# Kernel optimization log

Measured on AMD Instinct MI355X. Metric: run time of the kernel, lower is better.

The kernel has to match this reference:

```python
import jax, jax.numpy as jnp
import numpy as np

B, T, D, H, R = 8, 2048, 1024, 1024, 128
R_MAX, R_MIN, MAX_PHASE = 1.0, 0.0, 6.28


def setup_inputs() -> dict:
    key = jax.random.key(0)
    ks = jax.random.split(key, 10)
    x = jax.random.normal(ks[0], (B, T, D), dtype=jnp.float32)
    # nu_log / theta_log init as in the torch module constructor
    u1 = jax.random.uniform(ks[1], (H,), dtype=jnp.float32)
    inner = u1 * (R_MAX ** 2 - R_MIN ** 2) + R_MIN ** 2
    nu_log = jnp.log(-0.5 * jnp.log(inner + 1e-6) + 1e-6)
    u2 = jax.random.uniform(ks[2], (H,), dtype=jnp.float32)
    theta_log = jnp.log(MAX_PHASE * u2 + 1e-6)
    U1 = jax.random.normal(ks[3], (D, R), dtype=jnp.float32) / np.sqrt(D)
    U2 = jax.random.normal(ks[4], (D, R), dtype=jnp.float32) / np.sqrt(D)
    V1 = jax.random.normal(ks[5], (R, H), dtype=jnp.float32) / np.sqrt(R)
    V2 = jax.random.normal(ks[6], (R, H), dtype=jnp.float32) / np.sqrt(R)
    hc1_init = jax.random.normal(ks[7], (B, H), dtype=jnp.float32) * 0.1
    hc2_init = jax.random.normal(ks[8], (B, H), dtype=jnp.float32) * 0.1
    return {"x": x, "nu_log": nu_log, "theta_log": theta_log,
            "U1": U1, "U2": U2, "V1": V1, "V2": V2,
            "hc1_init": hc1_init, "hc2_init": hc2_init}


def _combine(left, right):
    # Compose complex rotations g+i*phi and accumulate rotated biases:
    # A = A_r * A_l ; b = A_r * b_l + b_r  (complex arithmetic in real pairs)
    gL, pL, bxL, byL = left
    gR, pR, bxR, byR = right
    g_new = gR * gL - pR * pL
    p_new = pR * gL + gR * pL
    bx_new = gR * bxL - pR * byL + bxR
    by_new = pR * bxL + gR * byL + byR
    return (g_new, p_new, bx_new, by_new)


def reference(x, nu_log, theta_log, U1, U2, V1, V2, hc1_init, hc2_init):
    r = jnp.exp(-jnp.exp(nu_log))                      # [H]
    theta = jnp.exp(theta_log)                         # [H]
    g = r * jnp.cos(theta)
    phi = r * jnp.sin(theta)
    gamma = jnp.sqrt(jnp.clip(1.0 - r * r, 0.0))
    # Low-rank input projections: [B,T,D] -> [B,T,R] -> [B,T,H]
    u1 = jnp.einsum('btr,rh->bth', jnp.einsum('btd,dr->btr', x, U1), V1)
    u2 = jnp.einsum('btr,rh->bth', jnp.einsum('btd,dr->btr', x, U2), V2)
    bx = u1 * gamma                                    # [B,T,H]
    by = u2 * gamma
    Bb, Tt, Hh = bx.shape
    gT = jnp.broadcast_to(g, (Bb, Tt, Hh))
    pT = jnp.broadcast_to(phi, (Bb, Tt, Hh))
    # Inclusive parallel scan over time (Hillis-Steele equivalent)
    gA, pA, Bx, By = jax.lax.associative_scan(_combine, (gT, pT, bx, by), axis=1)
    # c_t = A_t * c_0 + B_t  (complex mul in real pairs)
    c0x = hc1_init[:, None, :]
    c0y = hc2_init[:, None, :]
    c1 = gA * c0x - pA * c0y + Bx                      # [B,T,H]
    c2 = pA * c0x + gA * c0y + By
    # activation = identity (default nn.Identity in the module)
    y = jnp.concatenate([c1, c2], axis=-1)             # [B,T,2H]
    return y, c1[:, -1, :], c2[:, -1, :]
```

## Files before the change

kernel.cpp:

```cpp
#include <hip/hip_runtime.h>


using u16 = unsigned short;
using frag_ab = __attribute__((ext_vector_type(8))) short;
using frag_cd = __attribute__((ext_vector_type(4))) float;

__device__ __forceinline__ u16 f2bf(float f) {
    union { float f; unsigned u; } v; v.f = f;
    unsigned r = v.u + 0x7FFFu + ((v.u >> 16) & 1u);
    return (u16)(r >> 16);
}
__device__ __forceinline__ float bf2f(u16 s) {
    union { unsigned u; float f; } v; v.u = ((unsigned)s) << 16;
    return v.f;
}
__device__ __forceinline__ frag_cd mfma16(frag_ab a, frag_ab b, frag_cd c) {
    return __builtin_amdgcn_mfma_f32_16x16x32_bf16(a, b, c, 0, 0, 0);
}

__global__ __launch_bounds__(256) void k0_pack(
    const float* __restrict__ U1, const float* __restrict__ U2,
    const float* __restrict__ V1, const float* __restrict__ V2,
    u16* __restrict__ Ubfp, u16* __restrict__ Vt)
{
    int idx = blockIdx.x * 256 + threadIdx.x;
    if (idx < 32768) {
        int kg = idx & 127, n = idx >> 7;
        const float* Us = (n < 128) ? U1 : U2;
        int col = n & 127;
        u16 tmp[8];
#pragma unroll
        for (int j = 0; j < 8; ++j)
            tmp[j] = f2bf(Us[(size_t)(kg * 8 + j) * 128 + col]);
        *(uint4*)&Ubfp[((size_t)(kg >> 3) * 256 + n) * 64 + (kg & 7) * 8] = *(uint4*)tmp;
    } else {
        int i2 = idx - 32768;
        int kg = i2 & 15, h = (i2 >> 4) & 1023, br = i2 >> 14;
        const float* Vs = br ? V2 : V1;
        u16 tmp[8];
#pragma unroll
        for (int j = 0; j < 8; ++j)
            tmp[j] = f2bf(Vs[(size_t)(kg * 8 + j) * 1024 + h]);
        *(uint4*)&Vt[((size_t)br * 1024 + h) * 128 + kg * 8] = *(uint4*)tmp;
    }
}

__global__ __launch_bounds__(256) void k1_gemm(
    const float* __restrict__ x, const u16* __restrict__ Ubfp, u16* __restrict__ xu)
{
    __shared__ __align__(16) u16 Alds[4 * 520];
    __shared__ __align__(16) u16 Blds[32 * 520];
    u16* Tlds = Blds;
    const int tid = threadIdx.x;
    const int m0 = blockIdx.x * 32;
    const int wave = tid >> 6, lane = tid & 63;
    const int lm = lane & 15, q = lane >> 4;
    const int rowA = tid >> 3, kcA = tid & 7;
    frag_cd acc[2][4] = {};

    const float* xsrc = x + (size_t)(m0 + rowA) * 1024 + kcA * 8;
    const char* bsrc = (const char*)Ubfp;
    char* bdst = (char*)Blds;

    float4 pA0 = *(const float4*)xsrc;
    float4 pA1 = *(const float4*)(xsrc + 4);

    for (int kt = 0; kt < 16; ++kt) {
        {
            u16 ap[8] = { f2bf(pA0.x), f2bf(pA0.y), f2bf(pA0.z), f2bf(pA0.w),
                          f2bf(pA1.x), f2bf(pA1.y), f2bf(pA1.z), f2bf(pA1.w) };
            *(uint4*)&Alds[(rowA >> 3) * 520 + (rowA & 7) * 64 + kcA * 8] = *(uint4*)ap;
        }
#pragma unroll
        for (int i = 0; i < 8; ++i) {
            int blk = wave * 8 + i;
            __builtin_amdgcn_global_load_lds(
                (const __attribute__((address_space(1))) void*)(bsrc + (size_t)kt * 32768 + blk * 1024 + lane * 16),
                (__attribute__((address_space(3))) void*)(bdst + blk * 1040), 16, 0, 0);
        }
        __syncthreads();
        if (kt + 1 < 16) {
            pA0 = *(const float4*)(xsrc + (kt + 1) * 64);
            pA1 = *(const float4*)(xsrc + (kt + 1) * 64 + 4);
        }
        frag_ab a[2], b[4];
#pragma unroll
        for (int ksub = 0; ksub < 2; ++ksub) {
#pragma unroll
            for (int m4 = 0; m4 < 2; ++m4) {
                int ra = m4 * 16 + lm;
                a[m4] = *(const frag_ab*)&Alds[(ra >> 3) * 520 + (ra & 7) * 64 + ksub * 32 + q * 8];
            }
#pragma unroll
            for (int n4 = 0; n4 < 4; ++n4) {
                int nb = wave * 64 + n4 * 16 + lm;
                b[n4] = *(const frag_ab*)&Blds[(nb >> 3) * 520 + (nb & 7) * 64 + ksub * 32 + q * 8];
            }
#pragma unroll
            for (int m4 = 0; m4 < 2; ++m4)
#pragma unroll
                for (int n4 = 0; n4 < 4; ++n4)
                    acc[m4][n4] = mfma16(a[m4], b[n4], acc[m4][n4]);
        }
        __syncthreads();
    }
    const int rb = q * 4;
#pragma unroll
    for (int m4 = 0; m4 < 2; ++m4)
#pragma unroll
        for (int n4 = 0; n4 < 4; ++n4)
#pragma unroll
            for (int i = 0; i < 4; ++i) {
                int m = m4 * 16 + rb + i;
                int n = wave * 64 + n4 * 16 + lm;
                Tlds[m * 256 + n] = f2bf(acc[m4][n4][i]);
            }
    __syncthreads();
#pragma unroll
    for (int p = 0; p < 4; ++p) {
        int m = p * 8 + (tid >> 5);
        int c = tid & 31;
        uint4 v = *(const uint4*)&Tlds[m * 256 + c * 8];
        *(uint4*)&xu[(size_t)(m0 + m) * 256 + c * 8] = v;
    }
}

__device__ __forceinline__ void compute_u_tile(
    const u16* __restrict__ xu, const u16* __restrict__ Vt,
    int t0, int h0, int tid, u16* smem)
{
    u16* xulds = smem;
    u16* Vlds  = smem + 16640;
    const int wave = tid >> 6, lane = tid & 63;
    const int lm = lane & 15, q = lane >> 4;
    const int wrow = wave >> 1, wcol = wave & 1;

    const char* gsrc = (const char*)xu + (size_t)t0 * 512;
    char* lb = (char*)xulds;
#pragma unroll
    for (int i = 0; i < 8; ++i) {
        int blk = wave * 8 + i;
        __builtin_amdgcn_global_load_lds(
            (const __attribute__((address_space(1))) void*)(gsrc + blk * 1024 + lane * 16),
            (__attribute__((address_space(3))) void*)(lb + blk * 1040), 16, 0, 0);
    }

    const int nV = tid & 63, wV = tid >> 6;
    const int ra0 = wrow * 32 + lm, ra1 = ra0 + 16;
    const int ba0 = (ra0 >> 1) * 520 + (ra0 & 1) * 256;
    const int ba1 = (ra1 >> 1) * 520 + (ra1 & 1) * 256;
    const int nb0 = wcol * 32 + lm, nb1 = nb0 + 16;
    frag_cd acc[2][2][2] = {};
#pragma unroll
    for (int br = 0; br < 2; ++br) {
#pragma unroll
        for (int ii = 0; ii < 4; ++ii) {
            int g = wV * 4 + ii;
            uint4 v = *(const uint4*)&Vt[((size_t)br * 1024 + h0 + nV) * 128 + g * 8];
            *(uint4*)&Vlds[nV * 128 + (g ^ (nV & 15)) * 8] = v;
        }
        __syncthreads();
#pragma unroll
        for (int ks = 0; ks < 4; ++ks) {
            int koff = br * 128 + ks * 32 + q * 8;
            frag_ab a0 = *(const frag_ab*)&xulds[ba0 + koff];
            frag_ab a1 = *(const frag_ab*)&xulds[ba1 + koff];
            int gb = ks * 4 + q;
            frag_ab b0 = *(const frag_ab*)&Vlds[nb0 * 128 + (gb ^ (nb0 & 15)) * 8];
            frag_ab b1 = *(const frag_ab*)&Vlds[nb1 * 128 + (gb ^ (nb1 & 15)) * 8];
            acc[br][0][0] = mfma16(a0, b0, acc[br][0][0]);
            acc[br][0][1] = mfma16(a0, b1, acc[br][0][1]);
            acc[br][1][0] = mfma16(a1, b0, acc[br][1][0]);
            acc[br][1][1] = mfma16(a1, b1, acc[br][1][1]);
        }
        __syncthreads();
    }
    const int rb = q * 4;
#pragma unroll
    for (int br = 0; br < 2; ++br)
#pragma unroll
        for (int fr = 0; fr < 2; ++fr)
#pragma unroll
            for (int fc = 0; fc < 2; ++fc)
#pragma unroll
                for (int i = 0; i < 4; ++i) {
                    int tt = wrow * 32 + fr * 16 + rb + i;
                    int hh = wcol * 32 + fc * 16 + lm;
                    smem[br * 4352 + tt * 68 + hh] = f2bf(acc[br][fr][fc][i]);
                }
    __syncthreads();
}

__device__ __forceinline__ void lambda_of(const float* nu_log, const float* theta_log,
                                          int h, float& g, float& ph, float& gam)
{
    float rr = expf(-expf(nu_log[h]));
    float th = expf(theta_log[h]);
    g = rr * cosf(th);
    ph = rr * sinf(th);
    gam = sqrtf(fmaxf(1.0f - rr * rr, 0.0f));
}

__global__ __launch_bounds__(256, 3) void k2_agg(
    const u16* __restrict__ xu, const u16* __restrict__ Vt,
    const float* __restrict__ nu_log, const float* __restrict__ theta_log,
    float2* __restrict__ agg)
{
    __shared__ __align__(16) u16 smem[24832];
    const int tid = threadIdx.x;
    const int h0 = blockIdx.x * 64;
    const int t0 = blockIdx.y * 64;
    compute_u_tile(xu, Vt, t0, h0, tid, smem);

    const int hl = tid & 63, sc = tid >> 6;
    const int h = h0 + hl;
    float g, ph, gam;
    lambda_of(nu_log, theta_log, h, g, ph, gam);
    float bx = 0.f, by = 0.f;
#pragma unroll
    for (int j = 0; j < 16; ++j) {
        int tt = sc * 16 + j;
        float u1 = bf2f(smem[tt * 68 + hl]);
        float u2 = bf2f(smem[4352 + tt * 68 + hl]);
        float ex = gam * u1, ey = gam * u2;
        float nx = fmaf(g, bx, fmaf(-ph, by, ex));
        float ny = fmaf(ph, bx, fmaf(g, by, ey));
        bx = nx; by = ny;
    }
    const int b = t0 >> 11;
    const int nc = ((t0 & 2047) >> 4) + sc;
    agg[((size_t)b * 128 + nc) * 1024 + h] = make_float2(bx, by);
}

__global__ __launch_bounds__(64) void k3_scan(
    float2* __restrict__ agg_carry, const float* __restrict__ nu_log,
    const float* __restrict__ theta_log, const float* __restrict__ hc1,
    const float* __restrict__ hc2)
{
    const int idx = blockIdx.x * 64 + threadIdx.x;
    const int b = idx >> 10, h = idx & 1023;
    float g, ph, gam;
    lambda_of(nu_log, theta_log, h, g, ph, gam);
    float ax = g, ay = ph;
#pragma unroll
    for (int i = 0; i < 4; ++i) { float nx = ax * ax - ay * ay, ny = 2.f * ax * ay; ax = nx; ay = ny; }
    float cx = hc1[idx], cy = hc2[idx];
    float2* acp = agg_carry + (size_t)b * 128 * 1024 + h;
#pragma unroll 8
    for (int c = 0; c < 128; ++c) {
        float2 a = acp[(size_t)c * 1024];
        acp[(size_t)c * 1024] = make_float2(cx, cy);
        float nx = fmaf(ax, cx, fmaf(-ay, cy, a.x));
        float ny = fmaf(ay, cx, fmaf(ax, cy, a.y));
        cx = nx; cy = ny;
    }
}

__global__ __launch_bounds__(256, 3) void k4_apply(
    const u16* __restrict__ xu, const u16* __restrict__ Vt,
    const float* __restrict__ nu_log, const float* __restrict__ theta_log,
    const float2* __restrict__ carries, float* __restrict__ out)
{
    __shared__ __align__(16) u16 smem[24832];
    const int tid = threadIdx.x;
    const int h0 = blockIdx.x * 64;
    const int t0 = blockIdx.y * 64;
    compute_u_tile(xu, Vt, t0, h0, tid, smem);

    const int hl = tid & 63, sc = tid >> 6;
    const int h = h0 + hl;
    float g, ph, gam;
    lambda_of(nu_log, theta_log, h, g, ph, gam);
    const int b = t0 >> 11;
    const int tloc = t0 & 2047;
    const int nc = (tloc >> 4) + sc;
    float2 cin = carries[((size_t)b * 128 + nc) * 1024 + h];
    float cx = cin.x, cy = cin.y;
    float* yb = out + (size_t)b * (2048 * 2048);
#pragma unroll
    for (int j = 0; j < 16; ++j) {
        int tt = sc * 16 + j;
        float u1 = bf2f(smem[tt * 68 + hl]);
        float u2 = bf2f(smem[4352 + tt * 68 + hl]);
        float ex = gam * u1, ey = gam * u2;
        float nx = fmaf(g, cx, fmaf(-ph, cy, ex));
        float ny = fmaf(ph, cx, fmaf(g, cy, ey));
        cx = nx; cy = ny;
        int t = tloc + tt;
        yb[(size_t)t * 2048 + h] = cx;
        yb[(size_t)t * 2048 + 1024 + h] = cy;
    }
    if (tloc + sc * 16 == 2032) {
        out[(size_t)33554432 + (size_t)b * 1024 + h] = cx;
        out[(size_t)33554432 + 8192 + (size_t)b * 1024 + h] = cy;
    }
}

extern "C" void kernel_launch(void* const* d_in, const int* in_sizes, int n_in,
                              void* d_out, int out_size, void* d_ws, size_t ws_size,
                              hipStream_t stream) {
    const float* x         = (const float*)d_in[0];
    const float* nu_log    = (const float*)d_in[1];
    const float* theta_log = (const float*)d_in[2];
    const float* U1        = (const float*)d_in[3];
    const float* U2        = (const float*)d_in[4];
    const float* V1        = (const float*)d_in[5];
    const float* V2        = (const float*)d_in[6];
    const float* hc1       = (const float*)d_in[7];
    const float* hc2       = (const float*)d_in[8];

    u16*    xu   = (u16*)d_ws;
    float2* agg  = (float2*)((char*)d_ws + (size_t)8 * 1024 * 1024);
    u16*    Vt   = (u16*)((char*)d_ws + (size_t)16 * 1024 * 1024);
    u16*    Ubfp = (u16*)((char*)d_ws + (size_t)16 * 1024 * 1024 + 512 * 1024);

    k0_pack<<<256, 256, 0, stream>>>(U1, U2, V1, V2, Ubfp, Vt);
    k1_gemm<<<512, 256, 0, stream>>>(x, Ubfp, xu);
    k2_agg<<<dim3(16, 256), 256, 0, stream>>>(xu, Vt, nu_log, theta_log, agg);
    k3_scan<<<128, 64, 0, stream>>>(agg, nu_log, theta_log, hc1, hc2);
    k4_apply<<<dim3(16, 256), 256, 0, stream>>>(xu, Vt, nu_log, theta_log, agg, (float*)d_out);
}
```

Measured before the change: 278.5 us.

## Cache bf16 u tiles from aggregate pass and reuse them in apply kernel

The aggregate kernel now writes its computed bf16 u tile (XOR-swizzled in shared memory instead of padded) to a workspace buffer. The apply kernel no longer recomputes the low-rank projection GEMM. It bulk-loads the cached tiles straight into LDS with global_load_lds and processes 256 timesteps by 4 hidden units per thread, using float4 output stores. This removes the duplicated MFMA work in the apply pass at the cost of extra workspace traffic (32 MB write plus read).

```diff
diff --git a/kernel.cpp b/kernel.cpp
--- a/kernel.cpp
+++ b/kernel.cpp
@@ -17,6 +17,7 @@
 __device__ __forceinline__ frag_cd mfma16(frag_ab a, frag_ab b, frag_cd c) {
     return __builtin_amdgcn_mfma_f32_16x16x32_bf16(a, b, c, 0, 0, 0);
 }
+__device__ __forceinline__ int ukey(int tt) { return (((tt >> 2) ^ (tt >> 4)) & 3) << 4; }
 
 __global__ __launch_bounds__(256) void k0_pack(
     const float* __restrict__ U1, const float* __restrict__ U2,
@@ -186,7 +187,7 @@
                 for (int i = 0; i < 4; ++i) {
                     int tt = wrow * 32 + fr * 16 + rb + i;
                     int hh = wcol * 32 + fc * 16 + lm;
-                    smem[br * 4352 + tt * 68 + hh] = f2bf(acc[br][fr][fc][i]);
+                    smem[br * 4096 + tt * 64 + (hh ^ ukey(tt))] = f2bf(acc[br][fr][fc][i]);
                 }
     __syncthreads();
 }
@@ -204,7 +205,7 @@
 __global__ __launch_bounds__(256, 3) void k2_agg(
     const u16* __restrict__ xu, const u16* __restrict__ Vt,
     const float* __restrict__ nu_log, const float* __restrict__ theta_log,
-    float2* __restrict__ agg)
+    float2* __restrict__ agg, u16* __restrict__ u_ws)
 {
     __shared__ __align__(16) u16 smem[24832];
     const int tid = threadIdx.x;
@@ -212,6 +213,15 @@
     const int t0 = blockIdx.y * 64;
     compute_u_tile(xu, Vt, t0, h0, tid, smem);
 
+    {
+        size_t tbase = ((size_t)blockIdx.y * 16 + blockIdx.x) * 8192;
+#pragma unroll
+        for (int i = 0; i < 4; ++i) {
+            uint4 v = *(const uint4*)&smem[(size_t)(i * 256 + tid) * 8];
+            *(uint4*)&u_ws[tbase + (size_t)(i * 256 + tid) * 8] = v;
+        }
+    }
+
     const int hl = tid & 63, sc = tid >> 6;
     const int h = h0 + hl;
     float g, ph, gam;
@@ -220,8 +230,9 @@
 #pragma unroll
     for (int j = 0; j < 16; ++j) {
         int tt = sc * 16 + j;
-        float u1 = bf2f(smem[tt * 68 + hl]);
-        float u2 = bf2f(smem[4352 + tt * 68 + hl]);
+        int off = tt * 64 + (hl ^ ukey(tt));
+        float u1 = bf2f(smem[off]);
+        float u2 = bf2f(smem[4096 + off]);
         float ex = gam * u1, ey = gam * u2;
         float nx = fmaf(g, bx, fmaf(-ph, by, ex));
         float ny = fmaf(ph, bx, fmaf(g, by, ey));
@@ -256,43 +267,71 @@
     }
 }
 
-__global__ __launch_bounds__(256, 3) void k4_apply(
-    const u16* __restrict__ xu, const u16* __restrict__ Vt,
+__global__ __launch_bounds__(256) void k4_apply(
+    const u16* __restrict__ u_ws,
     const float* __restrict__ nu_log, const float* __restrict__ theta_log,
     const float2* __restrict__ carries, float* __restrict__ out)
 {
-    __shared__ __align__(16) u16 smem[24832];
+    __shared__ __align__(16) u16 smem[32768];
     const int tid = threadIdx.x;
     const int h0 = blockIdx.x * 64;
-    const int t0 = blockIdx.y * 64;
-    compute_u_tile(xu, Vt, t0, h0, tid, smem);
-
-    const int hl = tid & 63, sc = tid >> 6;
-    const int h = h0 + hl;
-    float g, ph, gam;
-    lambda_of(nu_log, theta_log, h, g, ph, gam);
-    const int b = t0 >> 11;
-    const int tloc = t0 & 2047;
+    const int t0 = blockIdx.y * 256;
+    const int wave = tid >> 6, lane = tid & 63;
+    const char* gbase = (const char*)u_ws;
+    char* lbase = (char*)smem;
+#pragma unroll
+    for (int s = 0; s < 4; ++s) {
+        size_t tIdx = (size_t)((t0 >> 6) + s) * 16 + blockIdx.x;
+#pragma unroll
+        for (int i = 0; i < 4; ++i) {
+            int blk = wave * 4 + i;
+            __builtin_amdgcn_global_load_lds(
+                (const __attribute__((address_space(1))) void*)(gbase + tIdx * 16384 + blk * 1024 + lane * 16),
+                (__attribute__((address_space(3))) void*)(lbase + s * 16384 + blk * 1024 + lane * 16), 16, 0, 0);
+        }
+    }
+
+    const int hg = tid & 15, sc = tid >> 4;
+    const int h = h0 + hg * 4;
+    const int b = t0 >> 11, tloc = t0 & 2047;
     const int nc = (tloc >> 4) + sc;
-    float2 cin = carries[((size_t)b * 128 + nc) * 1024 + h];
-    float cx = cin.x, cy = cin.y;
+    float g[4], ph[4], gam[4];
+#pragma unroll
+    for (int k = 0; k < 4; ++k) lambda_of(nu_log, theta_log, h + k, g[k], ph[k], gam[k]);
+    const float2* cp = carries + ((size_t)b * 128 + nc) * 1024 + h;
+    float4 cab = *(const float4*)cp;
+    float4 ccd = *(const float4*)(cp + 2);
+    float cx[4] = { cab.x, cab.z, ccd.x, ccd.z };
+    float cy[4] = { cab.y, cab.w, ccd.y, ccd.w };
     float* yb = out + (size_t)b * (2048 * 2048);
+    __syncthreads();
+
 #pragma unroll
     for (int j = 0; j < 16; ++j) {
         int tt = sc * 16 + j;
-        float u1 = bf2f(smem[tt * 68 + hl]);
-        float u2 = bf2f(smem[4352 + tt * 68 + hl]);
-        float ex = gam * u1, ey = gam * u2;
-        float nx = fmaf(g, cx, fmaf(-ph, cy, ex));
-        float ny = fmaf(ph, cx, fmaf(g, cy, ey));
-        cx = nx; cy = ny;
+        int s = tt >> 6, t6 = tt & 63;
+        int off = s * 8192 + t6 * 64 + ((hg * 4) ^ ukey(t6));
+        uint2 r1 = *(const uint2*)&smem[off];
+        uint2 r2 = *(const uint2*)&smem[off + 4096];
+        u16 a1[4]; *(uint2*)a1 = r1;
+        u16 a2[4]; *(uint2*)a2 = r2;
+#pragma unroll
+        for (int k = 0; k < 4; ++k) {
+            float u1 = bf2f(a1[k]), u2 = bf2f(a2[k]);
+            float ex = gam[k] * u1, ey = gam[k] * u2;
+            float nx = fmaf(g[k], cx[k], fmaf(-ph[k], cy[k], ex));
+            float ny = fmaf(ph[k], cx[k], fmaf(g[k], cy[k], ey));
+            cx[k] = nx; cy[k] = ny;
+        }
         int t = tloc + tt;
-        yb[(size_t)t * 2048 + h] = cx;
-        yb[(size_t)t * 2048 + 1024 + h] = cy;
+        *(float4*)&yb[(size_t)t * 2048 + h]        = make_float4(cx[0], cx[1], cx[2], cx[3]);
+        *(float4*)&yb[(size_t)t * 2048 + 1024 + h] = make_float4(cy[0], cy[1], cy[2], cy[3]);
     }
     if (tloc + sc * 16 == 2032) {
-        out[(size_t)33554432 + (size_t)b * 1024 + h] = cx;
-        out[(size_t)33554432 + 8192 + (size_t)b * 1024 + h] = cy;
+        *(float4*)&out[(size_t)33554432 + (size_t)b * 1024 + h] =
+            make_float4(cx[0], cx[1], cx[2], cx[3]);
+        *(float4*)&out[(size_t)33554432 + 8192 + (size_t)b * 1024 + h] =
+            make_float4(cy[0], cy[1], cy[2], cy[3]);
     }
 }
 
@@ -313,10 +352,11 @@
     float2* agg  = (float2*)((char*)d_ws + (size_t)8 * 1024 * 1024);
     u16*    Vt   = (u16*)((char*)d_ws + (size_t)16 * 1024 * 1024);
     u16*    Ubfp = (u16*)((char*)d_ws + (size_t)16 * 1024 * 1024 + 512 * 1024);
+    u16*    u_ws = (u16*)((char*)d_ws + (size_t)17 * 1024 * 1024);
 
     k0_pack<<<256, 256, 0, stream>>>(U1, U2, V1, V2, Ubfp, Vt);
     k1_gemm<<<512, 256, 0, stream>>>(x, Ubfp, xu);
-    k2_agg<<<dim3(16, 256), 256, 0, stream>>>(xu, Vt, nu_log, theta_log, agg);
+    k2_agg<<<dim3(16, 256), 256, 0, stream>>>(xu, Vt, nu_log, theta_log, agg, u_ws);
     k3_scan<<<128, 64, 0, stream>>>(agg, nu_log, theta_log, hc1, hc2);
-    k4_apply<<<dim3(16, 256), 256, 0, stream>>>(xu, Vt, nu_log, theta_log, agg, (float*)d_out);
-}
+    k4_apply<<<dim3(16, 64), 256, 0, stream>>>(u_ws, nu_log, theta_log, agg, (float*)d_out);
+}
```

Measured after the change: 281.2 us. About the same (+1.0%).

## Fuse low-rank GEMMs with chunk aggregation and store u once for apply

Applied to the files above, without the earlier changes.

Merges the x·U projection kernel and the per-chunk aggregation kernel into one fused kernel. Each block keeps its 32-row xu tile in LDS, computes u = xu·V for every H chunk, emits the chunk aggregates, and writes the bf16 u tile to a workspace buffer. The apply kernel then reads the precomputed u instead of redoing the second GEMM, and Vt is stored pre-swizzled so it can be copied straight into LDS. This removes the xu round trip and the duplicated u GEMM in exchange for an extra 64MB bf16 u write and read, plus lower occupancy and serialized work inside the fused kernel.

```diff
diff --git a/kernel.cpp b/kernel.cpp
--- a/kernel.cpp
+++ b/kernel.cpp
@@ -16,6 +16,15 @@
 }
 __device__ __forceinline__ frag_cd mfma16(frag_ab a, frag_ab b, frag_cd c) {
     return __builtin_amdgcn_mfma_f32_16x16x32_bf16(a, b, c, 0, 0, 0);
+}
+__device__ __forceinline__ void lambda_of(const float* nu_log, const float* theta_log,
+                                          int h, float& g, float& ph, float& gam)
+{
+    float rr = expf(-expf(nu_log[h]));
+    float th = expf(theta_log[h]);
+    g = rr * cosf(th);
+    ph = rr * sinf(th);
+    gam = sqrtf(fmaxf(1.0f - rr * rr, 0.0f));
 }
 
 __global__ __launch_bounds__(256) void k0_pack(
@@ -41,26 +50,26 @@
 #pragma unroll
         for (int j = 0; j < 8; ++j)
             tmp[j] = f2bf(Vs[(size_t)(kg * 8 + j) * 1024 + h]);
-        *(uint4*)&Vt[((size_t)br * 1024 + h) * 128 + kg * 8] = *(uint4*)tmp;
-    }
-}
-
-__global__ __launch_bounds__(256) void k1_gemm(
-    const float* __restrict__ x, const u16* __restrict__ Ubfp, u16* __restrict__ xu)
-{
-    __shared__ __align__(16) u16 Alds[4 * 520];
-    __shared__ __align__(16) u16 Blds[32 * 520];
-    u16* Tlds = Blds;
+        *(uint4*)&Vt[((size_t)br * 1024 + h) * 128 + (kg ^ (h & 15)) * 8] = *(uint4*)tmp;
+    }
+}
+
+__global__ __launch_bounds__(256, 2) void kB_fused(
+    const float* __restrict__ x, const u16* __restrict__ Ubfp, const u16* __restrict__ Vt,
+    const float* __restrict__ nu_log, const float* __restrict__ theta_log,
+    float2* __restrict__ agg, u16* __restrict__ u_ws)
+{
+    __shared__ __align__(16) u16 smem[24576];
     const int tid = threadIdx.x;
-    const int m0 = blockIdx.x * 32;
+    const int t0 = blockIdx.x * 32;
     const int wave = tid >> 6, lane = tid & 63;
     const int lm = lane & 15, q = lane >> 4;
+    char* smb = (char*)smem;
+
     const int rowA = tid >> 3, kcA = tid & 7;
-    frag_cd acc[2][4] = {};
-
-    const float* xsrc = x + (size_t)(m0 + rowA) * 1024 + kcA * 8;
+    frag_cd acc1[2][4] = {};
+    const float* xsrc = x + (size_t)(t0 + rowA) * 1024 + kcA * 8;
     const char* bsrc = (const char*)Ubfp;
-    char* bdst = (char*)Blds;
 
     float4 pA0 = *(const float4*)xsrc;
     float4 pA1 = *(const float4*)(xsrc + 4);
@@ -69,14 +78,14 @@
         {
             u16 ap[8] = { f2bf(pA0.x), f2bf(pA0.y), f2bf(pA0.z), f2bf(pA0.w),
                           f2bf(pA1.x), f2bf(pA1.y), f2bf(pA1.z), f2bf(pA1.w) };
-            *(uint4*)&Alds[(rowA >> 3) * 520 + (rowA & 7) * 64 + kcA * 8] = *(uint4*)ap;
+            *(uint4*)&smem[16640 + (rowA >> 3) * 520 + (rowA & 7) * 64 + kcA * 8] = *(uint4*)ap;
         }
 #pragma unroll
         for (int i = 0; i < 8; ++i) {
             int blk = wave * 8 + i;
             __builtin_amdgcn_global_load_lds(
                 (const __attribute__((address_space(1))) void*)(bsrc + (size_t)kt * 32768 + blk * 1024 + lane * 16),
-                (__attribute__((address_space(3))) void*)(bdst + blk * 1040), 16, 0, 0);
+                (__attribute__((address_space(3))) void*)(smb + blk * 1040), 16, 0, 0);
         }
         __syncthreads();
         if (kt + 1 < 16) {
@@ -87,149 +96,113 @@
 #pragma unroll
         for (int ksub = 0; ksub < 2; ++ksub) {
 #pragma unroll
-            for (int m4 = 0; m4 < 2; ++m4) {
-                int ra = m4 * 16 + lm;
-                a[m4] = *(const frag_ab*)&Alds[(ra >> 3) * 520 + (ra & 7) * 64 + ksub * 32 + q * 8];
+            for (int m2 = 0; m2 < 2; ++m2) {
+                int ra = m2 * 16 + lm;
+                a[m2] = *(const frag_ab*)&smem[16640 + (ra >> 3) * 520 + (ra & 7) * 64 + ksub * 32 + q * 8];
             }
 #pragma unroll
             for (int n4 = 0; n4 < 4; ++n4) {
                 int nb = wave * 64 + n4 * 16 + lm;
-                b[n4] = *(const frag_ab*)&Blds[(nb >> 3) * 520 + (nb & 7) * 64 + ksub * 32 + q * 8];
-            }
-#pragma unroll
-            for (int m4 = 0; m4 < 2; ++m4)
+                b[n4] = *(const frag_ab*)&smem[(nb >> 3) * 520 + (nb & 7) * 64 + ksub * 32 + q * 8];
+            }
+#pragma unroll
+            for (int m2 = 0; m2 < 2; ++m2)
 #pragma unroll
                 for (int n4 = 0; n4 < 4; ++n4)
-                    acc[m4][n4] = mfma16(a[m4], b[n4], acc[m4][n4]);
-        }
-        __syncthreads();
-    }
-    const int rb = q * 4;
-#pragma unroll
-    for (int m4 = 0; m4 < 2; ++m4)
+                    acc1[m2][n4] = mfma16(a[m2], b[n4], acc1[m2][n4]);
+        }
+        __syncthreads();
+    }
+#pragma unroll
+    for (int m2 = 0; m2 < 2; ++m2)
 #pragma unroll
         for (int n4 = 0; n4 < 4; ++n4)
 #pragma unroll
             for (int i = 0; i < 4; ++i) {
-                int m = m4 * 16 + rb + i;
-                int n = wave * 64 + n4 * 16 + lm;
-                Tlds[m * 256 + n] = f2bf(acc[m4][n4][i]);
+                int t = m2 * 16 + q * 4 + i;
+                int col = wave * 64 + n4 * 16 + lm;
+                int gcol = col >> 3;
+                int swz = (gcol & 16) | ((gcol ^ t) & 15);
+                smem[t * 256 + swz * 8 + (col & 7)] = f2bf(acc1[m2][n4][i]);
             }
     __syncthreads();
-#pragma unroll
-    for (int p = 0; p < 4; ++p) {
-        int m = p * 8 + (tid >> 5);
-        int c = tid & 31;
-        uint4 v = *(const uint4*)&Tlds[m * 256 + c * 8];
-        *(uint4*)&xu[(size_t)(m0 + m) * 256 + c * 8] = v;
-    }
-}
-
-__device__ __forceinline__ void compute_u_tile(
-    const u16* __restrict__ xu, const u16* __restrict__ Vt,
-    int t0, int h0, int tid, u16* smem)
-{
-    u16* xulds = smem;
-    u16* Vlds  = smem + 16640;
-    const int wave = tid >> 6, lane = tid & 63;
-    const int lm = lane & 15, q = lane >> 4;
-    const int wrow = wave >> 1, wcol = wave & 1;
-
-    const char* gsrc = (const char*)xu + (size_t)t0 * 512;
-    char* lb = (char*)xulds;
-#pragma unroll
-    for (int i = 0; i < 8; ++i) {
-        int blk = wave * 8 + i;
-        __builtin_amdgcn_global_load_lds(
-            (const __attribute__((address_space(1))) void*)(gsrc + blk * 1024 + lane * 16),
-            (__attribute__((address_space(3))) void*)(lb + blk * 1040), 16, 0, 0);
-    }
-
-    const int nV = tid & 63, wV = tid >> 6;
-    const int ra0 = wrow * 32 + lm, ra1 = ra0 + 16;
-    const int ba0 = (ra0 >> 1) * 520 + (ra0 & 1) * 256;
-    const int ba1 = (ra1 >> 1) * 520 + (ra1 & 1) * 256;
-    const int nb0 = wcol * 32 + lm, nb1 = nb0 + 16;
-    frag_cd acc[2][2][2] = {};
-#pragma unroll
-    for (int br = 0; br < 2; ++br) {
-#pragma unroll
-        for (int ii = 0; ii < 4; ++ii) {
-            int g = wV * 4 + ii;
-            uint4 v = *(const uint4*)&Vt[((size_t)br * 1024 + h0 + nV) * 128 + g * 8];
-            *(uint4*)&Vlds[nV * 128 + (g ^ (nV & 15)) * 8] = v;
-        }
-        __syncthreads();
-#pragma unroll
-        for (int ks = 0; ks < 4; ++ks) {
-            int koff = br * 128 + ks * 32 + q * 8;
-            frag_ab a0 = *(const frag_ab*)&xulds[ba0 + koff];
-            frag_ab a1 = *(const frag_ab*)&xulds[ba1 + koff];
-            int gb = ks * 4 + q;
-            frag_ab b0 = *(const frag_ab*)&Vlds[nb0 * 128 + (gb ^ (nb0 & 15)) * 8];
-            frag_ab b1 = *(const frag_ab*)&Vlds[nb1 * 128 + (gb ^ (nb1 & 15)) * 8];
-            acc[br][0][0] = mfma16(a0, b0, acc[br][0][0]);
-            acc[br][0][1] = mfma16(a0, b1, acc[br][0][1]);
-            acc[br][1][0] = mfma16(a1, b0, acc[br][1][0]);
-            acc[br][1][1] = mfma16(a1, b1, acc[br][1][1]);
-        }
-        __syncthreads();
-    }
-    const int rb = q * 4;
-#pragma unroll
-    for (int br = 0; br < 2; ++br)
-#pragma unroll
-        for (int fr = 0; fr < 2; ++fr)
-#pragma unroll
-            for (int fc = 0; fc < 2; ++fc)
-#pragma unroll
-                for (int i = 0; i < 4; ++i) {
-                    int tt = wrow * 32 + fr * 16 + rb + i;
-                    int hh = wcol * 32 + fc * 16 + lm;
-                    smem[br * 4352 + tt * 68 + hh] = f2bf(acc[br][fr][fc][i]);
-                }
-    __syncthreads();
-}
-
-__device__ __forceinline__ void lambda_of(const float* nu_log, const float* theta_log,
-                                          int h, float& g, float& ph, float& gam)
-{
-    float rr = expf(-expf(nu_log[h]));
-    float th = expf(theta_log[h]);
-    g = rr * cosf(th);
-    ph = rr * sinf(th);
-    gam = sqrtf(fmaxf(1.0f - rr * rr, 0.0f));
-}
-
-__global__ __launch_bounds__(256, 3) void k2_agg(
-    const u16* __restrict__ xu, const u16* __restrict__ Vt,
-    const float* __restrict__ nu_log, const float* __restrict__ theta_log,
-    float2* __restrict__ agg)
-{
-    __shared__ __align__(16) u16 smem[24832];
-    const int tid = threadIdx.x;
-    const int h0 = blockIdx.x * 64;
-    const int t0 = blockIdx.y * 64;
-    compute_u_tile(xu, Vt, t0, h0, tid, smem);
-
-    const int hl = tid & 63, sc = tid >> 6;
-    const int h = h0 + hl;
-    float g, ph, gam;
-    lambda_of(nu_log, theta_log, h, g, ph, gam);
-    float bx = 0.f, by = 0.f;
-#pragma unroll
-    for (int j = 0; j < 16; ++j) {
-        int tt = sc * 16 + j;
-        float u1 = bf2f(smem[tt * 68 + hl]);
-        float u2 = bf2f(smem[4352 + tt * 68 + hl]);
-        float ex = gam * u1, ey = gam * u2;
-        float nx = fmaf(g, bx, fmaf(-ph, by, ex));
-        float ny = fmaf(ph, bx, fmaf(g, by, ey));
-        bx = nx; by = ny;
-    }
+
+    const int hl = tid & 127, sc = tid >> 7;
     const int b = t0 >> 11;
-    const int nc = ((t0 & 2047) >> 4) + sc;
-    agg[((size_t)b * 128 + nc) * 1024 + h] = make_float2(bx, by);
+    const int ncb = (t0 & 2047) >> 4;
+
+    for (int c = 0; c < 8; ++c) {
+        frag_cd acc2[2][2][2] = {};
+#pragma unroll
+        for (int br = 0; br < 2; ++br) {
+            const char* vsrc = (const char*)Vt + ((size_t)br * 1024 + c * 128) * 256;
+#pragma unroll
+            for (int i = 0; i < 8; ++i) {
+                int blk = wave * 8 + i;
+                __builtin_amdgcn_global_load_lds(
+                    (const __attribute__((address_space(1))) void*)(vsrc + blk * 1024 + lane * 16),
+                    (__attribute__((address_space(3))) void*)(smb + 16384 + blk * 1024 + lane * 16), 16, 0, 0);
+            }
+            __syncthreads();
+#pragma unroll
+            for (int ks = 0; ks < 4; ++ks) {
+                int gk = br * 16 + ks * 4 + q;
+                int ra0 = lm, ra1 = 16 + lm;
+                frag_ab a0 = *(const frag_ab*)&smem[ra0 * 256 + ((gk & 16) | ((gk ^ ra0) & 15)) * 8];
+                frag_ab a1 = *(const frag_ab*)&smem[ra1 * 256 + ((gk & 16) | ((gk ^ ra1) & 15)) * 8];
+                int gv = ks * 4 + q;
+                int nb0 = wave * 32 + lm, nb1 = nb0 + 16;
+                frag_ab b0 = *(const frag_ab*)&smem[8192 + nb0 * 128 + ((gv ^ (nb0 & 15)) * 8)];
+                frag_ab b1 = *(const frag_ab*)&smem[8192 + nb1 * 128 + ((gv ^ (nb1 & 15)) * 8)];
+                acc2[br][0][0] = mfma16(a0, b0, acc2[br][0][0]);
+                acc2[br][0][1] = mfma16(a0, b1, acc2[br][0][1]);
+                acc2[br][1][0] = mfma16(a1, b0, acc2[br][1][0]);
+                acc2[br][1][1] = mfma16(a1, b1, acc2[br][1][1]);
+            }
+            __syncthreads();
+        }
+#pragma unroll
+        for (int br = 0; br < 2; ++br)
+#pragma unroll
+            for (int m2 = 0; m2 < 2; ++m2)
+#pragma unroll
+                for (int n2 = 0; n2 < 2; ++n2)
+#pragma unroll
+                    for (int i = 0; i < 4; ++i) {
+                        int t = m2 * 16 + q * 4 + i;
+                        int hloc = wave * 32 + n2 * 16 + lm;
+                        int sw = ((hloc >> 3) ^ (t & 15)) * 8 + (hloc & 7);
+                        smem[8192 + br * 4096 + t * 128 + sw] = f2bf(acc2[br][m2][n2][i]);
+                    }
+        __syncthreads();
+        {
+            int h = c * 128 + hl;
+            float g, ph, gam;
+            lambda_of(nu_log, theta_log, h, g, ph, gam);
+            float bx = 0.f, by = 0.f;
+#pragma unroll
+            for (int j = 0; j < 16; ++j) {
+                int tt = sc * 16 + j;
+                int sw = ((hl >> 3) ^ (tt & 15)) * 8 + (hl & 7);
+                float u1 = bf2f(smem[8192 + tt * 128 + sw]);
+                float u2 = bf2f(smem[8192 + 4096 + tt * 128 + sw]);
+                float ex = gam * u1, ey = gam * u2;
+                float nx = fmaf(g, bx, fmaf(-ph, by, ex));
+                float ny = fmaf(ph, bx, fmaf(g, by, ey));
+                bx = nx; by = ny;
+            }
+            agg[((size_t)b * 128 + ncb + sc) * 1024 + h] = make_float2(bx, by);
+        }
+        {
+            size_t ub = ((size_t)blockIdx.x * 8 + c) * 8192;
+#pragma unroll
+            for (int i = 0; i < 4; ++i) {
+                uint4 v = *(const uint4*)&smem[(size_t)8192 + (i * 256 + tid) * 8];
+                *(uint4*)&u_ws[ub + (size_t)(i * 256 + tid) * 8] = v;
+            }
+        }
+        __syncthreads();
+    }
 }
 
 __global__ __launch_bounds__(64) void k3_scan(
@@ -256,43 +229,48 @@
     }
 }
 
-__global__ __launch_bounds__(256, 3) void k4_apply(
-    const u16* __restrict__ xu, const u16* __restrict__ Vt,
+__global__ __launch_bounds__(256) void k4_apply(
+    const u16* __restrict__ u_ws,
     const float* __restrict__ nu_log, const float* __restrict__ theta_log,
     const float2* __restrict__ carries, float* __restrict__ out)
 {
-    __shared__ __align__(16) u16 smem[24832];
     const int tid = threadIdx.x;
-    const int h0 = blockIdx.x * 64;
-    const int t0 = blockIdx.y * 64;
-    compute_u_tile(xu, Vt, t0, h0, tid, smem);
-
-    const int hl = tid & 63, sc = tid >> 6;
-    const int h = h0 + hl;
+    const int c = blockIdx.x;
+    const int tb = blockIdx.y;
+    const int hl = tid & 127, sc2 = tid >> 7;
+    const int h = c * 128 + hl;
+    const int b = tb >> 5;
     float g, ph, gam;
     lambda_of(nu_log, theta_log, h, g, ph, gam);
-    const int b = t0 >> 11;
-    const int tloc = t0 & 2047;
-    const int nc = (tloc >> 4) + sc;
-    float2 cin = carries[((size_t)b * 128 + nc) * 1024 + h];
-    float cx = cin.x, cy = cin.y;
     float* yb = out + (size_t)b * (2048 * 2048);
 #pragma unroll
-    for (int j = 0; j < 16; ++j) {
-        int tt = sc * 16 + j;
-        float u1 = bf2f(smem[tt * 68 + hl]);
-        float u2 = bf2f(smem[4352 + tt * 68 + hl]);
-        float ex = gam * u1, ey = gam * u2;
-        float nx = fmaf(g, cx, fmaf(-ph, cy, ex));
-        float ny = fmaf(ph, cx, fmaf(g, cy, ey));
-        cx = nx; cy = ny;
-        int t = tloc + tt;
-        yb[(size_t)t * 2048 + h] = cx;
-        yb[(size_t)t * 2048 + 1024 + h] = cy;
-    }
-    if (tloc + sc * 16 == 2032) {
-        out[(size_t)33554432 + (size_t)b * 1024 + h] = cx;
-        out[(size_t)33554432 + 8192 + (size_t)b * 1024 + h] = cy;
+    for (int s = 0; s < 2; ++s) {
+        int seg = sc2 * 2 + s;
+        int nc = (tb & 31) * 4 + seg;
+        int tbase = (tb & 31) * 64 + seg * 16;
+        float2 cin = carries[((size_t)b * 128 + nc) * 1024 + h];
+        float cx = cin.x, cy = cin.y;
+        int tb32 = tb * 2 + (seg >> 1);
+        int ttb = (seg & 1) * 16;
+        const u16* ut = u_ws + ((size_t)tb32 * 8 + c) * 8192;
+#pragma unroll
+        for (int j = 0; j < 16; ++j) {
+            int tt = ttb + j;
+            int sw = ((hl >> 3) ^ (tt & 15)) * 8 + (hl & 7);
+            float u1 = bf2f(ut[tt * 128 + sw]);
+            float u2 = bf2f(ut[4096 + tt * 128 + sw]);
+            float ex = gam * u1, ey = gam * u2;
+            float nx = fmaf(g, cx, fmaf(-ph, cy, ex));
+            float ny = fmaf(ph, cx, fmaf(g, cy, ey));
+            cx = nx; cy = ny;
+            int t = tbase + j;
+            yb[(size_t)t * 2048 + h] = cx;
+            yb[(size_t)t * 2048 + 1024 + h] = cy;
+        }
+        if ((tb & 31) == 31 && seg == 3) {
+            out[(size_t)33554432 + (size_t)b * 1024 + h] = cx;
+            out[(size_t)33554432 + 8192 + (size_t)b * 1024 + h] = cy;
+        }
     }
 }
 
@@ -309,14 +287,13 @@
     const float* hc1       = (const float*)d_in[7];
     const float* hc2       = (const float*)d_in[8];
 
-    u16*    xu   = (u16*)d_ws;
     float2* agg  = (float2*)((char*)d_ws + (size_t)8 * 1024 * 1024);
     u16*    Vt   = (u16*)((char*)d_ws + (size_t)16 * 1024 * 1024);
     u16*    Ubfp = (u16*)((char*)d_ws + (size_t)16 * 1024 * 1024 + 512 * 1024);
+    u16*    u_ws = (u16*)((char*)d_ws + (size_t)17 * 1024 * 1024);
 
     k0_pack<<<256, 256, 0, stream>>>(U1, U2, V1, V2, Ubfp, Vt);
-    k1_gemm<<<512, 256, 0, stream>>>(x, Ubfp, xu);
-    k2_agg<<<dim3(16, 256), 256, 0, stream>>>(xu, Vt, nu_log, theta_log, agg);
+    kB_fused<<<512, 256, 0, stream>>>(x, Ubfp, Vt, nu_log, theta_log, agg, u_ws);
     k3_scan<<<128, 64, 0, stream>>>(agg, nu_log, theta_log, hc1, hc2);
-    k4_apply<<<dim3(16, 256), 256, 0, stream>>>(xu, Vt, nu_log, theta_log, agg, (float*)d_out);
-}
+    k4_apply<<<dim3(8, 256), 256, 0, stream>>>(u_ws, nu_log, theta_log, agg, (float*)d_out);
+}
```

Measured after the change: 272.9 us. 1.02x faster.
